# Performance work log

Hardware: AMD Instinct MI355X
Metric: run time of the kernel (lower is better)

## Reference

```python
import jax, jax.numpy as jnp
import numpy as np

B = 262144
D_IN = 128
D_H = 128


def setup_inputs() -> dict:
    key = jax.random.key(0)
    ks = jax.random.split(key, 16)
    stdv = 1.0 / np.sqrt(D_H)

    def u(k, shape):
        return jax.random.uniform(k, shape, jnp.float32, -stdv, stdv)

    inp = {
        "x": jax.random.normal(ks[0], (B, D_IN), jnp.float32),
        "h_t": jax.random.normal(ks[1], (B, D_H), jnp.float32),
        "c_t": jax.random.normal(ks[2], (B, D_H), jnp.float32),
        # params, same shapes/init (uniform +-1/sqrt(H)) as the torch module
        "W_xi": u(ks[3], (D_IN, D_H)), "W_hi": u(ks[4], (D_H, D_H)), "b_i": u(ks[5], (D_H,)),
        "W_xf": u(ks[6], (D_IN, D_H)), "W_hf": u(ks[7], (D_H, D_H)), "b_f": u(ks[8], (D_H,)),
        "W_xc": u(ks[9], (D_IN, D_H)), "W_hc": u(ks[10], (D_H, D_H)), "b_c": u(ks[11], (D_H,)),
        "W_xo": u(ks[12], (D_IN, D_H)), "W_ho": u(ks[13], (D_H, D_H)), "b_o": u(ks[14], (D_H,)),
    }
    return inp


def reference(x, h_t, c_t,
              W_xi, W_hi, b_i,
              W_xf, W_hf, b_f,
              W_xc, W_hc, b_c,
              W_xo, W_ho, b_o):
    # Fuse the 8 small GEMMs into 2 by concatenating gate weights along the
    # output dim: [D, 4H]. Same math as 8 separate matmuls.
    W_x = jnp.concatenate([W_xi, W_xf, W_xc, W_xo], axis=1)  # [D_in, 4H]
    W_h = jnp.concatenate([W_hi, W_hf, W_hc, W_ho], axis=1)  # [H, 4H]
    b = jnp.concatenate([b_i, b_f, b_c, b_o], axis=0)        # [4H]

    gates = x @ W_x + h_t @ W_h + b                           # [B, 4H]
    gi, gf, gc, go = jnp.split(gates, 4, axis=1)
    i_t = jax.nn.sigmoid(gi)
    f_t = jax.nn.sigmoid(gf)
    g_t = jnp.tanh(gc)
    o_t = jax.nn.sigmoid(go)
    c_new = f_t * c_t + i_t * g_t
    h_new = o_t * jnp.tanh(c_new)
    # original returns (hidden_seq, (h_t, c_t)) with hidden_seq == h_t
    return (h_new, (h_new, c_new))
```

## Files before the change

kernel.cpp:

```cpp
#include <hip/hip_runtime.h>

#define DH 128
#define TR 32

typedef __attribute__((ext_vector_type(8))) short bf16x8;
typedef __attribute__((ext_vector_type(8))) unsigned short u16x8;
typedef __attribute__((ext_vector_type(4))) float f32x4;
typedef __attribute__((ext_vector_type(4))) int   i32x4;

__device__ inline unsigned rnd_bf16(float f){
  unsigned u = __builtin_bit_cast(unsigned, f);
  u += 0x7fffu + ((u >> 16) & 1u);
  return u;
}
__device__ inline int pk2(float a, float b){
  unsigned ua = rnd_bf16(a), ub = rnd_bf16(b);
  return (int)((ua >> 16) | (ub & 0xffff0000u));
}
__device__ inline float fsigmoid(float v){
  float e = __builtin_amdgcn_exp2f(v * -1.442695040888963f);
  return __builtin_amdgcn_rcpf(1.0f + e);
}
__device__ inline float ftanhf(float v){
  float e = __builtin_amdgcn_exp2f(v * 2.885390081777927f);
  return 1.0f - 2.0f * __builtin_amdgcn_rcpf(1.0f + e);
}

__global__ void prep_weights(const float* __restrict__ Wxi, const float* __restrict__ Whi, const float* __restrict__ bi,
                             const float* __restrict__ Wxf, const float* __restrict__ Whf, const float* __restrict__ bf_,
                             const float* __restrict__ Wxc, const float* __restrict__ Whc, const float* __restrict__ bc,
                             const float* __restrict__ Wxo, const float* __restrict__ Who, const float* __restrict__ bo,
                             u16x8* __restrict__ Wf, float* __restrict__ bcat){
  int gid  = blockIdx.x * 256 + threadIdx.x;
  int lane = gid & 63;
  int ks   = (gid >> 6) & 7;
  int t    = (gid >> 9) & 1;
  int g    = (gid >> 10) & 3;
  int hsv  = (gid >> 12) & 3;
  int l15 = lane & 15, lg = lane >> 4;
  int hcol = hsv * 32 + t * 16 + l15;
  int kb   = ks * 32 + lg * 8;
  const float* Wx = (g == 0) ? Wxi : (g == 1) ? Wxf : (g == 2) ? Wxc : Wxo;
  const float* Wh = (g == 0) ? Whi : (g == 1) ? Whf : (g == 2) ? Whc : Who;
  u16x8 o;
  #pragma unroll
  for (int j = 0; j < 8; ++j){
    int k = kb + j;
    float v = (k < 128) ? Wx[k * DH + hcol] : Wh[(k - 128) * DH + hcol];
    o[j] = (unsigned short)(rnd_bf16(v) >> 16);
  }
  Wf[gid] = o;
  if (gid < 512){
    int gg = gid >> 7, hc = gid & 127;
    const float* bp = (gg == 0) ? bi : (gg == 1) ? bf_ : (gg == 2) ? bc : bo;
    bcat[gid] = bp[hc];
  }
}

__global__ __launch_bounds__(512, 6)
void lstm_fused(const float* __restrict__ x, const float* __restrict__ hin,
                const float* __restrict__ cin, const bf16x8* __restrict__ Wf,
                const float* __restrict__ bcat, float* __restrict__ out, int Btot){
  __shared__ __attribute__((aligned(16))) unsigned char smem[32768];
  bf16x8* xh  = (bf16x8*)smem;
  float*  hls = (float*)smem;
  float*  cls = (float*)(smem + 16384);

  const int tid = threadIdx.x;
  const int l   = tid & 63;
  const int wid = tid >> 6;
  const int l15 = l & 15;
  const int lg  = l >> 4;
  const int col = wid * 16 + l15;
  const size_t rowb = (size_t)blockIdx.x * TR;

  const int srow = tid >> 4;
  const int sc   = tid & 15;
  const float* px = x   + (rowb + srow) * DH + sc * 8;
  const float* ph = hin + (rowb + srow) * DH + sc * 8;
  f32x4 x0 = __builtin_nontemporal_load((const f32x4*)(px));
  f32x4 x1 = __builtin_nontemporal_load((const f32x4*)(px + 4));
  f32x4 h0 = __builtin_nontemporal_load((const f32x4*)(ph));
  f32x4 h1 = __builtin_nontemporal_load((const f32x4*)(ph + 4));

  float cr[2][4];
  #pragma unroll
  for (int m = 0; m < 2; ++m)
    #pragma unroll
    for (int r = 0; r < 4; ++r)
      cr[m][r] = __builtin_nontemporal_load(
          cin + (rowb + m * 16 + lg * 4 + r) * DH + col);

  {
    const int sw = srow & 7;
    i32x4 p;
    p[0] = pk2(x0[0], x0[1]); p[1] = pk2(x0[2], x0[3]);
    p[2] = pk2(x1[0], x1[1]); p[3] = pk2(x1[2], x1[3]);
    xh[srow * 32 + ( sc       ^ sw)] = __builtin_bit_cast(bf16x8, p);
    p[0] = pk2(h0[0], h0[1]); p[1] = pk2(h0[2], h0[3]);
    p[2] = pk2(h1[0], h1[1]); p[3] = pk2(h1[2], h1[3]);
    xh[srow * 32 + ((16 + sc) ^ sw)] = __builtin_bit_cast(bf16x8, p);
  }
  __syncthreads();

  float bb[4];
  #pragma unroll
  for (int g = 0; g < 4; ++g)
    bb[g] = bcat[g * 128 + col];

  const bf16x8* wv = Wf + (size_t)(wid >> 1) * 4096 + l;
  const int tw = wid & 1;

  f32x4 acc[2][4];
  #pragma unroll
  for (int m = 0; m < 2; ++m)
    #pragma unroll
    for (int g = 0; g < 4; ++g)
      acc[m][g] = (f32x4){0.f, 0.f, 0.f, 0.f};

  #pragma unroll
  for (int ks = 0; ks < 8; ++ks){
    bf16x8 a[2];
    #pragma unroll
    for (int m = 0; m < 2; ++m){
      const int row = m * 16 + l15;
      a[m] = xh[row * 32 + ((ks * 4 + lg) ^ (row & 7))];
    }
    #pragma unroll
    for (int g = 0; g < 4; ++g){
      bf16x8 bw = wv[(((g * 2 + tw) * 8) + ks) * 64];
      acc[0][g] = __builtin_amdgcn_mfma_f32_16x16x32_bf16(a[0], bw, acc[0][g], 0, 0, 0);
      acc[1][g] = __builtin_amdgcn_mfma_f32_16x16x32_bf16(a[1], bw, acc[1][g], 0, 0, 0);
    }
  }
  __syncthreads();

  #pragma unroll
  for (int m = 0; m < 2; ++m){
    #pragma unroll
    for (int r = 0; r < 4; ++r){
      const int rl = m * 16 + lg * 4 + r;
      const int swp = (rl & 7) << 2;
      float gi = acc[m][0][r] + bb[0];
      float gf = acc[m][1][r] + bb[1];
      float gc = acc[m][2][r] + bb[2];
      float go = acc[m][3][r] + bb[3];
      float i_t = fsigmoid(gi);
      float f_t = fsigmoid(gf);
      float g_t = ftanhf(gc);
      float o_t = fsigmoid(go);
      float cn = f_t * cr[m][r] + i_t * g_t;
      float hn = o_t * ftanhf(cn);
      hls[rl * DH + (col ^ swp)] = hn;
      cls[rl * DH + (col ^ swp)] = cn;
    }
  }
  __syncthreads();

  const size_t o1 = (size_t)Btot * DH;
  const int wcol = (l & 31) * 4;
  #pragma unroll
  for (int j = 0; j < 2; ++j){
    const int row = wid * 4 + j * 2 + (l >> 5);
    const int sw2 = (row & 7) << 2;
    f32x4 vh = *(const f32x4*)&hls[row * DH + (wcol ^ sw2)];
    f32x4 vc = *(const f32x4*)&cls[row * DH + (wcol ^ sw2)];
    float* po = out + (rowb + row) * DH + wcol;
    __builtin_nontemporal_store(vh, (f32x4*)(po));
    __builtin_nontemporal_store(vh, (f32x4*)(po + o1));
    __builtin_nontemporal_store(vc, (f32x4*)(po + 2 * o1));
  }
}

extern "C" void kernel_launch(void* const* d_in, const int* in_sizes, int n_in,
                              void* d_out, int out_size, void* d_ws, size_t ws_size,
                              hipStream_t stream){
  const float* x  = (const float*)d_in[0];
  const float* ht = (const float*)d_in[1];
  const float* ct = (const float*)d_in[2];
  u16x8* Wf   = (u16x8*)d_ws;
  float* bcat = (float*)((char*)d_ws + 16384 * 16);
  const int Btot = in_sizes[0] / DH;

  prep_weights<<<64, 256, 0, stream>>>(
      (const float*)d_in[3],  (const float*)d_in[4],  (const float*)d_in[5],
      (const float*)d_in[6],  (const float*)d_in[7],  (const float*)d_in[8],
      (const float*)d_in[9],  (const float*)d_in[10], (const float*)d_in[11],
      (const float*)d_in[12], (const float*)d_in[13], (const float*)d_in[14],
      Wf, bcat);

  lstm_fused<<<Btot / TR, 512, 0, stream>>>(x, ht, ct, (const bf16x8*)Wf, bcat,
                                            (float*)d_out, Btot);
}
```

Baseline: 255.4 us.

## Prefetch first weight slices early, split LDS buffers, drop a barrier

The first two k-slices of bf16 weights are now loaded into registers before the x/h conversion, so their global latency overlaps the input staging. The input and output LDS buffers are separated, which makes the barrier between the MFMA loop and the epilogue writes unnecessary, so it is removed. The output stores are regrouped so all LDS reads finish before the streaming stores are issued. In exchange, LDS per block grows from 32 KB to 48 KB and register use rises, which may limit how many blocks fit on a CU at the requested occupancy.

```diff
diff --git a/kernel.cpp b/kernel.cpp
--- a/kernel.cpp
+++ b/kernel.cpp
@@ -61,10 +61,9 @@
 void lstm_fused(const float* __restrict__ x, const float* __restrict__ hin,
                 const float* __restrict__ cin, const bf16x8* __restrict__ Wf,
                 const float* __restrict__ bcat, float* __restrict__ out, int Btot){
-  __shared__ __attribute__((aligned(16))) unsigned char smem[32768];
-  bf16x8* xh  = (bf16x8*)smem;
-  float*  hls = (float*)smem;
-  float*  cls = (float*)(smem + 16384);
+  __shared__ __attribute__((aligned(16))) bf16x8 xh[TR * 32];
+  __shared__ __attribute__((aligned(16))) float  hls[TR * DH];
+  __shared__ __attribute__((aligned(16))) float  cls[TR * DH];
 
   const int tid = threadIdx.x;
   const int l   = tid & 63;
@@ -90,6 +89,15 @@
     for (int r = 0; r < 4; ++r)
       cr[m][r] = __builtin_nontemporal_load(
           cin + (rowb + m * 16 + lg * 4 + r) * DH + col);
+
+  const bf16x8* wv = Wf + (size_t)(wid >> 1) * 4096 + l;
+  const int tw = wid & 1;
+  bf16x8 bwA[4], bwB[4];
+  #pragma unroll
+  for (int g = 0; g < 4; ++g){
+    bwA[g] = wv[(((g * 2 + tw) * 8) + 0) * 64];
+    bwB[g] = wv[(((g * 2 + tw) * 8) + 1) * 64];
+  }
 
   {
     const int sw = srow & 7;
@@ -108,9 +116,6 @@
   for (int g = 0; g < 4; ++g)
     bb[g] = bcat[g * 128 + col];
 
-  const bf16x8* wv = Wf + (size_t)(wid >> 1) * 4096 + l;
-  const int tw = wid & 1;
-
   f32x4 acc[2][4];
   #pragma unroll
   for (int m = 0; m < 2; ++m)
@@ -128,12 +133,13 @@
     }
     #pragma unroll
     for (int g = 0; g < 4; ++g){
-      bf16x8 bw = wv[(((g * 2 + tw) * 8) + ks) * 64];
+      bf16x8 bw = (ks == 0) ? bwA[g]
+                : (ks == 1) ? bwB[g]
+                : wv[(((g * 2 + tw) * 8) + ks) * 64];
       acc[0][g] = __builtin_amdgcn_mfma_f32_16x16x32_bf16(a[0], bw, acc[0][g], 0, 0, 0);
       acc[1][g] = __builtin_amdgcn_mfma_f32_16x16x32_bf16(a[1], bw, acc[1][g], 0, 0, 0);
     }
   }
-  __syncthreads();
 
   #pragma unroll
   for (int m = 0; m < 2; ++m){
@@ -159,17 +165,25 @@
 
   const size_t o1 = (size_t)Btot * DH;
   const int wcol = (l & 31) * 4;
+  f32x4 vh[2], vc[2];
+  int rows[2];
   #pragma unroll
   for (int j = 0; j < 2; ++j){
     const int row = wid * 4 + j * 2 + (l >> 5);
     const int sw2 = (row & 7) << 2;
-    f32x4 vh = *(const f32x4*)&hls[row * DH + (wcol ^ sw2)];
-    f32x4 vc = *(const f32x4*)&cls[row * DH + (wcol ^ sw2)];
-    float* po = out + (rowb + row) * DH + wcol;
-    __builtin_nontemporal_store(vh, (f32x4*)(po));
-    __builtin_nontemporal_store(vh, (f32x4*)(po + o1));
-    __builtin_nontemporal_store(vc, (f32x4*)(po + 2 * o1));
-  }
+    rows[j] = row;
+    vh[j] = *(const f32x4*)&hls[row * DH + (wcol ^ sw2)];
+    vc[j] = *(const f32x4*)&cls[row * DH + (wcol ^ sw2)];
+  }
+  #pragma unroll
+  for (int j = 0; j < 2; ++j)
+    __builtin_nontemporal_store(vh[j], (f32x4*)(out + (rowb + rows[j]) * DH + wcol));
+  #pragma unroll
+  for (int j = 0; j < 2; ++j)
+    __builtin_nontemporal_store(vh[j], (f32x4*)(out + o1 + (rowb + rows[j]) * DH + wcol));
+  #pragma unroll
+  for (int j = 0; j < 2; ++j)
+    __builtin_nontemporal_store(vc[j], (f32x4*)(out + 2 * o1 + (rowb + rows[j]) * DH + wcol));
 }
 
 extern "C" void kernel_launch(void* const* d_in, const int* in_sizes, int n_in,
```

New measurement: 326.5 us. 27.9% more time.
